# Kernel optimization log

Measured on AMD Instinct MI355X. Metric: run time of the kernel, lower is better.

The kernel has to match this reference:

```python
import jax, jax.numpy as jnp
import numpy as np

EPS = 1e-8            # torch cosine_similarity eps
RECENCY_WEIGHT = 0.3  # retrieve() default
NOVELTY_SCALE = 10.0  # _compute_novelty divides min dist by 10

B, N, D, K = 32, 1_000_000, 128, 16


def setup_inputs() -> dict:
    key = jax.random.key(0)
    ks = jax.random.split(key, 6)
    query = jax.random.normal(ks[0], (B, D), dtype=jnp.float32)
    memory = jax.random.normal(ks[1], (N, D), dtype=jnp.float32)
    importance = jax.random.uniform(ks[2], (N,), dtype=jnp.float32)
    timestamps = jnp.sort(jax.random.randint(ks[3], (N,), 0, N).astype(jnp.int32))
    Wq = jax.random.normal(ks[4], (D, D), dtype=jnp.float32) / jnp.sqrt(jnp.float32(D))
    bq = jax.random.normal(ks[5], (D,), dtype=jnp.float32) * 0.01
    return {
        "query": query,
        "memory": memory,
        "importance": importance,
        "timestamps": timestamps,
        "Wq": Wq,
        "bq": bq,
        "current_time": N,
        "k": K,
    }


def reference(query, memory, importance, timestamps, Wq, bq, current_time, k):
    # query_net: Linear(item_dim, item_dim)
    q = query @ Wq.T + bq                              # [B, D]

    # --- batched cosine similarity against the whole bank (replaces Python loop) ---
    q_norm = jnp.sqrt(jnp.sum(q * q, axis=-1, keepdims=True))          # [B, 1]
    m_norm = jnp.sqrt(jnp.sum(memory * memory, axis=-1, keepdims=True))  # [N, 1]
    dots = jnp.einsum("bd,nd->bn", q, memory)                          # [B, N]
    sim = dots / jnp.maximum(q_norm * m_norm.T, EPS)                   # [B, N]

    # recency = (timestamp + 1) / (current_time + 1)
    recency = (timestamps.astype(jnp.float32) + 1.0) / (jnp.float32(current_time) + 1.0)  # [N]

    score = (1.0 - RECENCY_WEIGHT) * sim + RECENCY_WEIGHT * recency[None, :]
    score = score * (0.5 + 0.5 * importance)[None, :]                  # [B, N]

    topk_scores, topk_idx = jax.lax.top_k(score, k)                    # [B, k]

    # --- novelty: min L2 distance from q to any stored vector, capped at 1 ---
    # ||q - m||^2 = ||q||^2 + ||m||^2 - 2 q.m
    d2 = q_norm**2 + m_norm.T**2 - 2.0 * dots                          # [B, N]
    min_dist = jnp.sqrt(jnp.maximum(jnp.min(d2, axis=-1), 0.0))        # [B]
    novelty = jnp.minimum(1.0, min_dist / NOVELTY_SCALE)               # [B]

    return topk_scores, topk_idx, novelty
```

## Files before the change

### kernel.cpp

```cpp
#include <hip/hip_runtime.h>
#include <float.h>

#define BQ 32
#define DIM 128
#define TOPK 16
#define G1 768
#define T1 256
#define T2 256
#define NCAND (G1*16)

__global__ void ph0_qproj(const float* __restrict__ query, const float* __restrict__ Wq,
                          const float* __restrict__ bq,
                          float* __restrict__ qT, float* __restrict__ qn2,
                          float* __restrict__ sinvq)
{
    const int b = blockIdx.x;
    const int d = threadIdx.x;
    float s = bq[d];
    #pragma unroll 8
    for (int kk = 0; kk < DIM; ++kk)
        s = fmaf(query[b * DIM + kk], Wq[d * DIM + kk], s);
    qT[d * BQ + b] = s;
    __shared__ float red[DIM];
    red[d] = s * s;
    __syncthreads();
    for (int off = DIM / 2; off >= 1; off >>= 1) {
        if (d < off) red[d] += red[d + off];
        __syncthreads();
    }
    if (d == 0) {
        qn2[b] = red[0];
        sinvq[b] = 1.0f / sqrtf(red[0]);
    }
}

__global__ __launch_bounds__(T1, 3) void ph1_scan(
    const float* __restrict__ mem, const float* __restrict__ imp,
    const int* __restrict__ tsp, const float* __restrict__ qT,
    const float* __restrict__ sinvq, const float* __restrict__ qn2,
    const int* __restrict__ ctp,
    float* __restrict__ cand_sc, int* __restrict__ cand_ix,
    float* __restrict__ minD_ws, int N, int C, int iters)
{
    __shared__ float trbuf[4][64 * 36];

    const int tid = threadIdx.x;
    const int wave = tid >> 6;
    const int lane = tid & 63;
    const int g = blockIdx.x;
    const int n0 = g * C;
    const int n1 = (n0 + C < N) ? (n0 + C) : N;
    const int qsel = lane & 31;
    const int hsel = lane >> 5;

    const float invct = 1.0f / ((float)(*ctp) + 1.0f);
    const float sq = sinvq[qsel];
    const float qn2s = qn2[qsel];

    float top_s[TOPK];
    int   top_i[TOPK];
    #pragma unroll
    for (int j = 0; j < TOPK; ++j) { top_s[j] = -FLT_MAX; top_i[j] = 0; }
    float mind = FLT_MAX;

    float* tb = &trbuf[wave][0];

    for (int it = 0; it < iters; ++it) {
        const int rowbase = n0 + it * (4 * 64) + wave * 64;
        if (rowbase < n1) {
            const int row = rowbase + lane;
            const bool valid = row < n1;
            const int rc = valid ? row : (n1 - 1);
            const float4* mrow = (const float4*)(mem + (size_t)rc * DIM);

            float acc[BQ];
            #pragma unroll
            for (int b = 0; b < BQ; ++b) acc[b] = 0.0f;
            float m2 = 0.0f;

            float4 pf[4];
            #pragma unroll
            for (int j = 0; j < 4; ++j) pf[j] = mrow[j];

            #pragma unroll 1
            for (int dd = 0; dd < 8; ++dd) {
                #pragma unroll
                for (int jj = 0; jj < 4; ++jj) {
                    const int d4 = dd * 4 + jj;
                    float4 u = pf[jj];
                    const int nx = (d4 + 4 < 32) ? (d4 + 4) : 31;
                    pf[jj] = mrow[nx];
                    m2 = fmaf(u.x, u.x, fmaf(u.y, u.y, fmaf(u.z, u.z, fmaf(u.w, u.w, m2))));
                    const float* qp = qT + d4 * (4 * BQ);
                    #pragma unroll
                    for (int b = 0; b < BQ; ++b) acc[b] = fmaf(u.x, qp[b], acc[b]);
                    #pragma unroll
                    for (int b = 0; b < BQ; ++b) acc[b] = fmaf(u.y, qp[BQ + b], acc[b]);
                    #pragma unroll
                    for (int b = 0; b < BQ; ++b) acc[b] = fmaf(u.z, qp[2 * BQ + b], acc[b]);
                    #pragma unroll
                    for (int b = 0; b < BQ; ++b) acc[b] = fmaf(u.w, qp[3 * BQ + b], acc[b]);
                }
            }

            const float invm = rsqrtf(m2);
            const float recn = ((float)tsp[rc] + 1.0f) * invct;
            const float impf = fmaf(0.5f, imp[rc], 0.5f);
            const float k1 = 0.7f * invm * impf;
            const float k2 = 0.3f * recn * impf;

            #pragma unroll
            for (int b = 0; b < BQ; ++b) tb[lane * 36 + b] = acc[b];
            tb[lane * 36 + 32] = k1;
            tb[lane * 36 + 33] = k2;
            tb[lane * 36 + 34] = m2;
            tb[lane * 36 + 35] = valid ? 1.0f : -1.0f;

            #pragma unroll 1
            for (int j = 0; j < 32; ++j) {
                const int rr = (hsel << 5) + j;
                const float a = tb[rr * 36 + qsel];
                const float4 kk = *(const float4*)&tb[rr * 36 + 32];
                const float score = fmaf(a, kk.x * sq, kk.y);
                const float d2 = fmaf(-2.0f, a, qn2s + kk.z);
                if (kk.w > 0.0f) {
                    mind = fminf(mind, d2);
                    if (score > top_s[TOPK - 1]) {
                        float cs = score; int ci = rowbase + rr;
                        #pragma unroll
                        for (int p = 0; p < TOPK; ++p) {
                            const bool gt = cs > top_s[p];
                            const float tv = top_s[p]; const int tx = top_i[p];
                            top_s[p] = gt ? cs : tv;  top_i[p] = gt ? ci : tx;
                            cs = gt ? tv : cs;        ci = gt ? tx : ci;
                        }
                    }
                }
            }
        }
    }

    __syncthreads();
    float* dsc = &trbuf[0][0];
    int*   dix = (int*)(dsc + T1 * TOPK);
    float* dmn = dsc + 2 * T1 * TOPK;
    #pragma unroll
    for (int j = 0; j < TOPK; ++j) {
        dsc[tid * TOPK + j] = top_s[j];
        dix[tid * TOPK + j] = top_i[j];
    }
    dmn[tid] = mind;
    __syncthreads();

    for (int qq = 0; qq < 8; ++qq) {
        const int q = wave * 8 + qq;
        float sc2[2]; int ix2[2];
        #pragma unroll
        for (int s = 0; s < 2; ++s) {
            const int c = lane * 2 + s;
            const int L = (c >> 4) * 32 + q;
            const int slot = c & 15;
            sc2[s] = dsc[L * TOPK + slot];
            ix2[s] = dix[L * TOPK + slot];
        }
        float lm = (sc2[0] >= sc2[1]) ? sc2[0] : sc2[1];
        int   ls = (sc2[0] >= sc2[1]) ? 0 : 1;
        for (int r = 0; r < TOPK; ++r) {
            float v = lm; int we = lane;
            #pragma unroll
            for (int off = 32; off >= 1; off >>= 1) {
                const float ov = __shfl_xor(v, off);
                const int   oe = __shfl_xor(we, off);
                if (ov > v || (ov == v && oe < we)) { v = ov; we = oe; }
            }
            if (lane == we) {
                cand_sc[(g * 32 + q) * TOPK + r] = lm;
                cand_ix[(g * 32 + q) * TOPK + r] = ix2[ls];
                sc2[ls] = -FLT_MAX;
                lm = (sc2[0] >= sc2[1]) ? sc2[0] : sc2[1];
                ls = (sc2[0] >= sc2[1]) ? 0 : 1;
            }
        }
    }

    if (tid < 32) {
        float m = FLT_MAX;
        #pragma unroll
        for (int l = 0; l < 8; ++l) m = fminf(m, dmn[l * 32 + tid]);
        minD_ws[g * 32 + tid] = m;
    }
}

__global__ void ph2_final(const float* __restrict__ cand_sc, const int* __restrict__ cand_ix,
                          const float* __restrict__ minD_ws, float* __restrict__ out, int G)
{
    __shared__ float ssc[NCAND];
    __shared__ float shv[4];
    __shared__ int   she[4];
    __shared__ float smin[T2];

    const int q = blockIdx.x;
    const int tid = threadIdx.x;
    const int wave = tid >> 6;
    const int lane = tid & 63;

    for (int e = tid; e < NCAND; e += T2)
        ssc[e] = cand_sc[(e >> 4) * (32 * TOPK) + q * TOPK + (e & 15)];
    __syncthreads();

    float lm = ssc[tid]; int le = tid;
    for (int s = 1; s < NCAND / T2; ++s) {
        const int e = s * T2 + tid;
        const float v = ssc[e];
        if (v > lm) { lm = v; le = e; }
    }

    for (int r = 0; r < TOPK; ++r) {
        float v = lm; int e = le;
        #pragma unroll
        for (int off = 32; off >= 1; off >>= 1) {
            const float ov = __shfl_xor(v, off);
            const int   oe = __shfl_xor(e, off);
            if (ov > v || (ov == v && oe < e)) { v = ov; e = oe; }
        }
        if (lane == 0) { shv[wave] = v; she[wave] = e; }
        __syncthreads();
        float bv = shv[0]; int be = she[0];
        #pragma unroll
        for (int w2 = 1; w2 < 4; ++w2) {
            const float wv = shv[w2]; const int wе2 = she[w2];
            if (wv > bv || (wv == bv && wе2 < be)) { bv = wv; be = wе2; }
        }
        if (le == be) {
            out[q * TOPK + r] = bv;
            const int gix = cand_ix[(be >> 4) * (32 * TOPK) + q * TOPK + (be & 15)];
            out[BQ * TOPK + q * TOPK + r] = (float)gix;
            ssc[le] = -FLT_MAX;
            lm = ssc[tid]; le = tid;
            for (int s = 1; s < NCAND / T2; ++s) {
                const int e2 = s * T2 + tid;
                const float v2 = ssc[e2];
                if (v2 > lm) { lm = v2; le = e2; }
            }
        }
        __syncthreads();
    }

    float m = FLT_MAX;
    for (int g2 = tid; g2 < G; g2 += T2) m = fminf(m, minD_ws[g2 * 32 + q]);
    smin[tid] = m;
    __syncthreads();
    for (int off = T2 / 2; off >= 1; off >>= 1) {
        if (tid < off) smin[tid] = fminf(smin[tid], smin[tid + off]);
        __syncthreads();
    }
    if (tid == 0) {
        const float md = sqrtf(fmaxf(smin[0], 0.0f));
        out[2 * BQ * TOPK + q] = fminf(1.0f, md * 0.1f);
    }
}

extern "C" void kernel_launch(void* const* d_in, const int* in_sizes, int n_in,
                              void* d_out, int out_size, void* d_ws, size_t ws_size,
                              hipStream_t stream) {
    const float* query      = (const float*)d_in[0];
    const float* memory     = (const float*)d_in[1];
    const float* importance = (const float*)d_in[2];
    const int*   timestamps = (const int*)d_in[3];
    const float* Wq         = (const float*)d_in[4];
    const float* bq         = (const float*)d_in[5];
    const int*   ctp        = (const int*)d_in[6];
    const int N = in_sizes[2];

    float* ws      = (float*)d_ws;
    float* qT      = ws;
    float* qn2     = ws + 4096;
    float* sinvq   = ws + 4128;
    float* cand_sc = ws + 4352;
    int*   cand_ix = (int*)(ws + 4352 + G1 * 32 * TOPK);
    float* minD_ws = ws + 4352 + 2 * G1 * 32 * TOPK;

    const int C = (N + G1 - 1) / G1;
    const int iters = (C + (4 * 64) - 1) / (4 * 64);

    ph0_qproj<<<BQ, DIM, 0, stream>>>(query, Wq, bq, qT, qn2, sinvq);
    ph1_scan<<<G1, T1, 0, stream>>>(memory, importance, timestamps, qT, sinvq, qn2,
                                    ctp, cand_sc, cand_ix, minD_ws, N, C, iters);
    ph2_final<<<BQ, T2, 0, stream>>>(cand_sc, cand_ix, minD_ws, (float*)d_out, G1);
}
```

Before: 931.0 us.

## Register-block four rows per lane with LDS-staged query and grid-stride scan

Each lane now computes dot products for four memory rows at once, so every query value read from LDS is reused across four rows. The projected query is packed into float4 layout and staged in shared memory rather than read from global memory. Blocks grid-stride over 256-row units per wave, replacing contiguous chunks, with a larger grid sized against the workspace. This raises register pressure (128 accumulators), so launch bounds drop to 2 blocks per CU. The occupancy loss may offset the reduced LDS/global traffic per FMA.

```diff
diff --git a/kernel.cpp b/kernel.cpp
--- a/kernel.cpp
+++ b/kernel.cpp
@@ -4,14 +4,16 @@
 #define BQ 32
 #define DIM 128
 #define TOPK 16
-#define G1 768
 #define T1 256
 #define T2 256
-#define NCAND (G1*16)
+#define GBLK 992
+#define RPL 4
+#define UROWS (64*RPL)
+#define NCAND (GBLK*TOPK)
 
 __global__ void ph0_qproj(const float* __restrict__ query, const float* __restrict__ Wq,
                           const float* __restrict__ bq,
-                          float* __restrict__ qT, float* __restrict__ qn2,
+                          float* __restrict__ qpackf, float* __restrict__ qn2,
                           float* __restrict__ sinvq)
 {
     const int b = blockIdx.x;
@@ -20,7 +22,7 @@
     #pragma unroll 8
     for (int kk = 0; kk < DIM; ++kk)
         s = fmaf(query[b * DIM + kk], Wq[d * DIM + kk], s);
-    qT[d * BQ + b] = s;
+    qpackf[(d >> 2) * (BQ * 4) + b * 4 + (d & 3)] = s;
     __shared__ float red[DIM];
     red[d] = s * s;
     __syncthreads();
@@ -34,27 +36,35 @@
     }
 }
 
-__global__ __launch_bounds__(T1, 3) void ph1_scan(
+__global__ __launch_bounds__(T1, 2) void ph1_scan(
     const float* __restrict__ mem, const float* __restrict__ imp,
-    const int* __restrict__ tsp, const float* __restrict__ qT,
+    const int* __restrict__ tsp, const float* __restrict__ qpackg,
     const float* __restrict__ sinvq, const float* __restrict__ qn2,
     const int* __restrict__ ctp,
     float* __restrict__ cand_sc, int* __restrict__ cand_ix,
-    float* __restrict__ minD_ws, int N, int C, int iters)
+    float* __restrict__ minD_ws, int N, int wstride)
 {
-    __shared__ float trbuf[4][64 * 36];
-
-    const int tid = threadIdx.x;
+    __shared__ float smem[13312];
+
+    const int tid  = threadIdx.x;
     const int wave = tid >> 6;
     const int lane = tid & 63;
-    const int g = blockIdx.x;
-    const int n0 = g * C;
-    const int n1 = (n0 + C < N) ? (n0 + C) : N;
     const int qsel = lane & 31;
     const int hsel = lane >> 5;
+    const int g = blockIdx.x;
+
+    {
+        const float4* src = (const float4*)qpackg;
+        float4* dst = (float4*)smem;
+        #pragma unroll
+        for (int i = 0; i < 4; ++i) dst[tid + i * T1] = src[tid + i * T1];
+    }
+    __syncthreads();
+    const float4* qlds = (const float4*)smem;
+    float* tb = smem + 4096 + wave * (64 * 36);
 
     const float invct = 1.0f / ((float)(*ctp) + 1.0f);
-    const float sq = sinvq[qsel];
+    const float sq   = sinvq[qsel];
     const float qn2s = qn2[qsel];
 
     float top_s[TOPK];
@@ -63,59 +73,81 @@
     for (int j = 0; j < TOPK; ++j) { top_s[j] = -FLT_MAX; top_i[j] = 0; }
     float mind = FLT_MAX;
 
-    float* tb = &trbuf[wave][0];
-
-    for (int it = 0; it < iters; ++it) {
-        const int rowbase = n0 + it * (4 * 64) + wave * 64;
-        if (rowbase < n1) {
-            const int row = rowbase + lane;
-            const bool valid = row < n1;
-            const int rc = valid ? row : (n1 - 1);
-            const float4* mrow = (const float4*)(mem + (size_t)rc * DIM);
-
-            float acc[BQ];
+    const int units = (N + UROWS - 1) / UROWS;
+
+    for (int u = g * 4 + wave; u < units; u += wstride) {
+        const int rowbase = u * UROWS + lane;
+        int rows[RPL]; bool vld[RPL];
+        #pragma unroll
+        for (int s = 0; s < RPL; ++s) { rows[s] = rowbase + s * 64; vld[s] = rows[s] < N; }
+        const float4* mr0 = (const float4*)(mem + (size_t)(vld[0] ? rows[0] : N - 1) * DIM);
+        const float4* mr1 = (const float4*)(mem + (size_t)(vld[1] ? rows[1] : N - 1) * DIM);
+        const float4* mr2 = (const float4*)(mem + (size_t)(vld[2] ? rows[2] : N - 1) * DIM);
+        const float4* mr3 = (const float4*)(mem + (size_t)(vld[3] ? rows[3] : N - 1) * DIM);
+
+        float acc[RPL][BQ];
+        #pragma unroll
+        for (int s = 0; s < RPL; ++s)
             #pragma unroll
-            for (int b = 0; b < BQ; ++b) acc[b] = 0.0f;
-            float m2 = 0.0f;
-
-            float4 pf[4];
+            for (int b = 0; b < BQ; ++b) acc[s][b] = 0.0f;
+        float m2[RPL];
+        #pragma unroll
+        for (int s = 0; s < RPL; ++s) m2[s] = 0.0f;
+
+        float4 n0 = mr0[0], n1 = mr1[0], n2 = mr2[0], n3 = mr3[0];
+
+        #pragma unroll 1
+        for (int dq = 0; dq < DIM / 4; ++dq) {
+            const float4 u0 = n0, u1 = n1, u2 = n2, u3 = n3;
+            const int nq = (dq < DIM / 4 - 1) ? dq + 1 : dq;
+            n0 = mr0[nq]; n1 = mr1[nq]; n2 = mr2[nq]; n3 = mr3[nq];
+
+            m2[0] = fmaf(u0.x, u0.x, fmaf(u0.y, u0.y, fmaf(u0.z, u0.z, fmaf(u0.w, u0.w, m2[0]))));
+            m2[1] = fmaf(u1.x, u1.x, fmaf(u1.y, u1.y, fmaf(u1.z, u1.z, fmaf(u1.w, u1.w, m2[1]))));
+            m2[2] = fmaf(u2.x, u2.x, fmaf(u2.y, u2.y, fmaf(u2.z, u2.z, fmaf(u2.w, u2.w, m2[2]))));
+            m2[3] = fmaf(u3.x, u3.x, fmaf(u3.y, u3.y, fmaf(u3.z, u3.z, fmaf(u3.w, u3.w, m2[3]))));
+
             #pragma unroll
-            for (int j = 0; j < 4; ++j) pf[j] = mrow[j];
-
-            #pragma unroll 1
-            for (int dd = 0; dd < 8; ++dd) {
-                #pragma unroll
-                for (int jj = 0; jj < 4; ++jj) {
-                    const int d4 = dd * 4 + jj;
-                    float4 u = pf[jj];
-                    const int nx = (d4 + 4 < 32) ? (d4 + 4) : 31;
-                    pf[jj] = mrow[nx];
-                    m2 = fmaf(u.x, u.x, fmaf(u.y, u.y, fmaf(u.z, u.z, fmaf(u.w, u.w, m2))));
-                    const float* qp = qT + d4 * (4 * BQ);
-                    #pragma unroll
-                    for (int b = 0; b < BQ; ++b) acc[b] = fmaf(u.x, qp[b], acc[b]);
-                    #pragma unroll
-                    for (int b = 0; b < BQ; ++b) acc[b] = fmaf(u.y, qp[BQ + b], acc[b]);
-                    #pragma unroll
-                    for (int b = 0; b < BQ; ++b) acc[b] = fmaf(u.z, qp[2 * BQ + b], acc[b]);
-                    #pragma unroll
-                    for (int b = 0; b < BQ; ++b) acc[b] = fmaf(u.w, qp[3 * BQ + b], acc[b]);
-                }
-            }
-
-            const float invm = rsqrtf(m2);
-            const float recn = ((float)tsp[rc] + 1.0f) * invct;
-            const float impf = fmaf(0.5f, imp[rc], 0.5f);
-            const float k1 = 0.7f * invm * impf;
-            const float k2 = 0.3f * recn * impf;
-
+            for (int b = 0; b < BQ; ++b) {
+                const float4 qv = qlds[dq * BQ + b];
+                acc[0][b] = fmaf(u0.x, qv.x, acc[0][b]);
+                acc[0][b] = fmaf(u0.y, qv.y, acc[0][b]);
+                acc[0][b] = fmaf(u0.z, qv.z, acc[0][b]);
+                acc[0][b] = fmaf(u0.w, qv.w, acc[0][b]);
+                acc[1][b] = fmaf(u1.x, qv.x, acc[1][b]);
+                acc[1][b] = fmaf(u1.y, qv.y, acc[1][b]);
+                acc[1][b] = fmaf(u1.z, qv.z, acc[1][b]);
+                acc[1][b] = fmaf(u1.w, qv.w, acc[1][b]);
+                acc[2][b] = fmaf(u2.x, qv.x, acc[2][b]);
+                acc[2][b] = fmaf(u2.y, qv.y, acc[2][b]);
+                acc[2][b] = fmaf(u2.z, qv.z, acc[2][b]);
+                acc[2][b] = fmaf(u2.w, qv.w, acc[2][b]);
+                acc[3][b] = fmaf(u3.x, qv.x, acc[3][b]);
+                acc[3][b] = fmaf(u3.y, qv.y, acc[3][b]);
+                acc[3][b] = fmaf(u3.z, qv.z, acc[3][b]);
+                acc[3][b] = fmaf(u3.w, qv.w, acc[3][b]);
+            }
+        }
+
+        #pragma unroll 1
+        for (int s = 0; s < RPL; ++s) {
+            float k1, k2v, m2v;
+            if (vld[s]) {
+                const float invm = rsqrtf(m2[s]);
+                const float recn = ((float)tsp[rows[s]] + 1.0f) * invct;
+                const float impf = fmaf(0.5f, imp[rows[s]], 0.5f);
+                k1 = 0.7f * invm * impf;
+                k2v = 0.3f * recn * impf;
+                m2v = m2[s];
+            } else {
+                k1 = 0.0f; k2v = -FLT_MAX; m2v = 3.0e37f;
+            }
             #pragma unroll
-            for (int b = 0; b < BQ; ++b) tb[lane * 36 + b] = acc[b];
+            for (int b = 0; b < BQ; ++b) tb[lane * 36 + b] = acc[s][b];
             tb[lane * 36 + 32] = k1;
-            tb[lane * 36 + 33] = k2;
-            tb[lane * 36 + 34] = m2;
-            tb[lane * 36 + 35] = valid ? 1.0f : -1.0f;
-
+            tb[lane * 36 + 33] = k2v;
+            tb[lane * 36 + 34] = m2v;
+            tb[lane * 36 + 35] = 0.0f;
             #pragma unroll 1
             for (int j = 0; j < 32; ++j) {
                 const int rr = (hsel << 5) + j;
@@ -123,17 +155,15 @@
                 const float4 kk = *(const float4*)&tb[rr * 36 + 32];
                 const float score = fmaf(a, kk.x * sq, kk.y);
                 const float d2 = fmaf(-2.0f, a, qn2s + kk.z);
-                if (kk.w > 0.0f) {
-                    mind = fminf(mind, d2);
-                    if (score > top_s[TOPK - 1]) {
-                        float cs = score; int ci = rowbase + rr;
-                        #pragma unroll
-                        for (int p = 0; p < TOPK; ++p) {
-                            const bool gt = cs > top_s[p];
-                            const float tv = top_s[p]; const int tx = top_i[p];
-                            top_s[p] = gt ? cs : tv;  top_i[p] = gt ? ci : tx;
-                            cs = gt ? tv : cs;        ci = gt ? tx : ci;
-                        }
+                mind = fminf(mind, d2);
+                if (score > top_s[TOPK - 1]) {
+                    float cs = score; int ci = u * UROWS + s * 64 + rr;
+                    #pragma unroll
+                    for (int p = 0; p < TOPK; ++p) {
+                        const bool gt = cs > top_s[p];
+                        const float tv = top_s[p]; const int tx = top_i[p];
+                        top_s[p] = gt ? cs : tv;  top_i[p] = gt ? ci : tx;
+                        cs = gt ? tv : cs;        ci = gt ? tx : ci;
                     }
                 }
             }
@@ -141,7 +171,7 @@
     }
 
     __syncthreads();
-    float* dsc = &trbuf[0][0];
+    float* dsc = smem + 4096;
     int*   dix = (int*)(dsc + T1 * TOPK);
     float* dmn = dsc + 2 * T1 * TOPK;
     #pragma unroll
@@ -203,9 +233,10 @@
     const int tid = threadIdx.x;
     const int wave = tid >> 6;
     const int lane = tid & 63;
+    const int gcand = G * TOPK;
 
     for (int e = tid; e < NCAND; e += T2)
-        ssc[e] = cand_sc[(e >> 4) * (32 * TOPK) + q * TOPK + (e & 15)];
+        ssc[e] = (e < gcand) ? cand_sc[(e >> 4) * (32 * TOPK) + q * TOPK + (e & 15)] : -FLT_MAX;
     __syncthreads();
 
     float lm = ssc[tid]; int le = tid;
@@ -228,8 +259,8 @@
         float bv = shv[0]; int be = she[0];
         #pragma unroll
         for (int w2 = 1; w2 < 4; ++w2) {
-            const float wv = shv[w2]; const int wе2 = she[w2];
-            if (wv > bv || (wv == bv && wе2 < be)) { bv = wv; be = wе2; }
+            const float wv = shv[w2]; const int we2 = she[w2];
+            if (wv > bv || (wv == bv && we2 < be)) { bv = wv; be = we2; }
         }
         if (le == be) {
             out[q * TOPK + r] = bv;
@@ -272,19 +303,23 @@
     const int*   ctp        = (const int*)d_in[6];
     const int N = in_sizes[2];
 
+    const size_t ws_floats = ws_size / 4;
+    int gb = GBLK;
+    if (ws_floats < (size_t)4352 + (size_t)GBLK * 1056) {
+        gb = (int)((ws_floats - 4352) / 1056);
+        if (gb < 1) gb = 1;
+    }
+
     float* ws      = (float*)d_ws;
-    float* qT      = ws;
+    float* qpack   = ws;
     float* qn2     = ws + 4096;
     float* sinvq   = ws + 4128;
     float* cand_sc = ws + 4352;
-    int*   cand_ix = (int*)(ws + 4352 + G1 * 32 * TOPK);
-    float* minD_ws = ws + 4352 + 2 * G1 * 32 * TOPK;
-
-    const int C = (N + G1 - 1) / G1;
-    const int iters = (C + (4 * 64) - 1) / (4 * 64);
-
-    ph0_qproj<<<BQ, DIM, 0, stream>>>(query, Wq, bq, qT, qn2, sinvq);
-    ph1_scan<<<G1, T1, 0, stream>>>(memory, importance, timestamps, qT, sinvq, qn2,
-                                    ctp, cand_sc, cand_ix, minD_ws, N, C, iters);
-    ph2_final<<<BQ, T2, 0, stream>>>(cand_sc, cand_ix, minD_ws, (float*)d_out, G1);
+    int*   cand_ix = (int*)(ws + 4352 + (size_t)gb * 512);
+    float* minD_ws = ws + 4352 + 2 * (size_t)gb * 512;
+
+    ph0_qproj<<<BQ, DIM, 0, stream>>>(query, Wq, bq, qpack, qn2, sinvq);
+    ph1_scan<<<gb, T1, 0, stream>>>(memory, importance, timestamps, qpack, sinvq, qn2,
+                                    ctp, cand_sc, cand_ix, minD_ws, N, gb * 4);
+    ph2_final<<<BQ, T2, 0, stream>>>(cand_sc, cand_ix, minD_ws, (float*)d_out, gb);
 }
```

New measurement: 1.310 ms. +40.7%, slower.
